# Kernel optimization log

Measured on AMD Instinct MI355X. Metric: run time of the kernel, lower is better.

## Reference

```python
import jax, jax.numpy as jnp
import numpy as np

TOP_K = 2

def setup_inputs() -> dict:
    key = jax.random.key(0)
    ks = jax.random.split(key, 8)
    B, S, H, E, F = 4, 2048, 1024, 8, 2048  # F = hidden * expansion(2)
    scale_in = 0.02
    return {
        "x": jax.random.normal(ks[0], (B, S, H), dtype=jnp.float32),
        "router_w": jax.random.normal(ks[1], (H, E), dtype=jnp.float32) * scale_in,
        "router_b": jnp.zeros((E,), dtype=jnp.float32),
        "w1": jax.random.normal(ks[2], (E, H, F), dtype=jnp.float32) * scale_in,
        "b1": jnp.zeros((E, F), dtype=jnp.float32),
        "w2": jax.random.normal(ks[3], (E, F, H), dtype=jnp.float32) * scale_in,
        "b2": jnp.zeros((E, H), dtype=jnp.float32),
    }

def reference(x, router_w, router_b, w1, b1, w2, b2):
    B, S, H = x.shape
    E = router_b.shape[0]
    T = B * S
    flat = x.reshape(T, H)
    # Router + top-k gating (softmax over the k selected logits, as in torch code)
    logits = flat @ router_w + router_b                       # [T, E]
    topk_scores, topk_idx = jax.lax.top_k(logits, TOP_K)      # [T, k]
    probs = jax.nn.softmax(topk_scores, axis=-1)              # [T, k]
    # Dense gate matrix: gates[t, e] = prob if e selected for token t else 0
    gates = jnp.zeros((T, E), dtype=flat.dtype).at[
        jnp.arange(T)[:, None], topk_idx
    ].add(probs)                                              # [T, E]
    # Expert FFNs computed as batched GEMMs over the expert axis
    h = jax.nn.relu(jnp.einsum('td,edf->etf', flat, w1) + b1[:, None, :])  # [E, T, F]
    eout = jnp.einsum('etf,efd->etd', h, w2) + b2[:, None, :]              # [E, T, H]
    out = jnp.einsum('etd,te->td', eout, gates)                            # [T, H]
    return out.reshape(B, S, H)
```

## Files before the change

### kernel.cpp

```cpp
#include <hip/hip_runtime.h>
#include <hip/hip_bf16.h>

#define T_TOK 8192
#define HDIM 1024
#define FDIM 2048
#define NEXP 8
#define NASSIGN (T_TOK * 2)
#define ROWCAP (NASSIGN + 128)
#define NHB 64

typedef __bf16 bf16;
typedef __bf16 bf16x4 __attribute__((ext_vector_type(4)));
typedef __bf16 bf16x8 __attribute__((ext_vector_type(8)));
typedef float f32x4 __attribute__((ext_vector_type(4)));

__device__ __forceinline__ void gload_lds16(const void* g, void* l) {
    __builtin_amdgcn_global_load_lds(
        (const __attribute__((address_space(1))) void*)(uintptr_t)g,
        (__attribute__((address_space(3))) void*)(uintptr_t)l,
        16, 0, 0);
}

__global__ __launch_bounds__(256) void transpose_to_bf16(
    const float* __restrict__ in, bf16* __restrict__ out, int R, int C) {
    __shared__ float tile[64][68];
    int e = blockIdx.z;
    const float* inp = in + (size_t)e * R * C;
    bf16* outp = out + (size_t)e * R * C;
    int c0 = blockIdx.x * 64, r0 = blockIdx.y * 64;
    int tid = threadIdx.x;
    int tx = tid & 15, ty = tid >> 4;
#pragma unroll
    for (int i = 0; i < 4; i++) {
        int row = ty + i * 16;
        float4 v = *(const float4*)&inp[(size_t)(r0 + row) * C + c0 + tx * 4];
        *(float4*)&tile[row][tx * 4] = v;
    }
    __syncthreads();
#pragma unroll
    for (int i = 0; i < 2; i++) {
        int idx = tid + i * 256;
        int c = idx >> 3, seg = idx & 7;
        bf16x8 v;
#pragma unroll
        for (int j = 0; j < 8; j++) v[j] = (bf16)tile[seg * 8 + j][c];
        *(bf16x8*)&outp[(size_t)(c0 + c) * R + r0 + seg * 8] = v;
    }
}

__global__ __launch_bounds__(256) void router_kernel(
    const float* __restrict__ x, const float* __restrict__ rw,
    const float* __restrict__ rb, int* __restrict__ expert_pair,
    float2* __restrict__ gate_pair) {
    __shared__ float rwT[NEXP][HDIM];
    __shared__ float rbs[NEXP];
    int tid = threadIdx.x;
    for (int i = tid; i < HDIM * NEXP / 4; i += 256) {
        float4 v = ((const float4*)rw)[i];
        int h = i >> 1, e0 = (i & 1) * 4;
        rwT[e0 + 0][h] = v.x;
        rwT[e0 + 1][h] = v.y;
        rwT[e0 + 2][h] = v.z;
        rwT[e0 + 3][h] = v.w;
    }
    if (tid < NEXP) rbs[tid] = rb[tid];
    __syncthreads();
    int wave = tid >> 6, lane = tid & 63;
    int tbase = blockIdx.x * 32 + wave * 8;

    for (int tk = 0; tk < 8; tk++) {
        int t = tbase + tk;
        const float4* xt = (const float4*)(x + (size_t)t * HDIM);
        float p[NEXP];
#pragma unroll
        for (int e = 0; e < NEXP; e++) p[e] = 0.f;
#pragma unroll
        for (int it = 0; it < 4; it++) {
            float4 v = xt[it * 64 + lane];
            int h = (it * 64 + lane) * 4;
#pragma unroll
            for (int e = 0; e < NEXP; e++) {
                float4 wv = *(const float4*)&rwT[e][h];
                p[e] += v.x * wv.x + v.y * wv.y + v.z * wv.z + v.w * wv.w;
            }
        }
#pragma unroll
        for (int off = 32; off >= 1; off >>= 1) {
#pragma unroll
            for (int e = 0; e < NEXP; e++) p[e] += __shfl_xor(p[e], off, 64);
        }
        if (lane == 0) {
            float lg[NEXP];
#pragma unroll
            for (int e = 0; e < NEXP; e++) lg[e] = p[e] + rbs[e];
            int e0 = 0;
#pragma unroll
            for (int e = 1; e < NEXP; e++)
                if (lg[e] > lg[e0]) e0 = e;
            int e1 = -1;
#pragma unroll
            for (int e = 0; e < NEXP; e++) {
                if (e == e0) continue;
                if (e1 < 0 || lg[e] > lg[e1]) e1 = e;
            }
            float z = expf(lg[e1] - lg[e0]);
            expert_pair[t] = e0 | (e1 << 16);
            gate_pair[t] = make_float2(1.f / (1.f + z), z / (1.f + z));
        }
    }
}

__global__ __launch_bounds__(256) void hist_kernel(
    const int* __restrict__ expert_pair, int* __restrict__ hist) {
    int tid = threadIdx.x;
    int wave = tid >> 6, lane = tid & 63;
    int a = blockIdx.x * 256 + tid;
    int t = a >> 1, j = a & 1;
    int e = (expert_pair[t] >> (16 * j)) & 0xffff;
    __shared__ int wcnt[4][NEXP];
#pragma unroll
    for (int ee = 0; ee < NEXP; ee++) {
        unsigned long long m = __ballot(e == ee);
        if (lane == 0) wcnt[wave][ee] = __popcll(m);
    }
    __syncthreads();
    if (tid < NEXP)
        hist[blockIdx.x * NEXP + tid] =
            wcnt[0][tid] + wcnt[1][tid] + wcnt[2][tid] + wcnt[3][tid];
}

__global__ __launch_bounds__(256) void scan_kernel(
    const int* __restrict__ hist, int* __restrict__ start,
    int* __restrict__ cnt, int* __restrict__ offs) {
    __shared__ int h[NHB * NEXP];
    __shared__ int tot[NEXP];
    __shared__ int offsh[NEXP];
    int tid = threadIdx.x;
    for (int i = tid; i < NHB * NEXP; i += 256) h[i] = hist[i];
    __syncthreads();
    if (tid < NEXP) {
        int s = 0;
        for (int b = 0; b < NHB; b++) s += h[b * NEXP + tid];
        tot[tid] = s;
        cnt[tid] = s;
    }
    __syncthreads();
    if (tid == 0) {
        int o = 0;
        for (int e = 0; e < NEXP; e++) {
            offsh[e] = o;
            offs[e] = o;
            o += tot[e];
        }
    }
    __syncthreads();
    if (tid < NEXP) {
        int run = offsh[tid];
        for (int b = 0; b < NHB; b++) {
            start[b * NEXP + tid] = run;
            run += h[b * NEXP + tid];
        }
    }
}

__global__ __launch_bounds__(256) void scatter_kernel(
    const int* __restrict__ expert_pair, const float2* __restrict__ gate_pair,
    const int* __restrict__ start, int* __restrict__ perm,
    float* __restrict__ gatebuf, int* __restrict__ rowbuf) {
    int tid = threadIdx.x;
    int wave = tid >> 6, lane = tid & 63;
    int a = blockIdx.x * 256 + tid;
    int t = a >> 1, j = a & 1;
    int e = (expert_pair[t] >> (16 * j)) & 0xffff;
    float2 gp = gate_pair[t];
    float g = j ? gp.y : gp.x;
    __shared__ int wcnt[4][NEXP];
    int rankw = 0;
    unsigned long long below = (1ull << lane) - 1ull;
#pragma unroll
    for (int ee = 0; ee < NEXP; ee++) {
        unsigned long long m = __ballot(e == ee);
        if (lane == 0) wcnt[wave][ee] = __popcll(m);
        if (ee == e) rankw = __popcll(m & below);
    }
    __syncthreads();
    int cross = 0;
    for (int w = 0; w < wave; w++) cross += wcnt[w][e];
    int pos = start[blockIdx.x * NEXP + e] + cross + rankw;
    perm[pos] = t;
    gatebuf[pos] = g;
    rowbuf[a] = pos;
}

__global__ __launch_bounds__(256) void pack_kernel(
    const float* __restrict__ x, const int* __restrict__ perm,
    bf16* __restrict__ xg) {
    int r0 = blockIdx.x * 16;
    int wave = threadIdx.x >> 6, lane = threadIdx.x & 63;
#pragma unroll
    for (int i = 0; i < 4; i++) {
        int row = r0 + wave * 4 + i;
        int tok = perm[row];
        const float* src = x + (size_t)tok * HDIM;
        bf16* dst = xg + (size_t)row * HDIM;
#pragma unroll
        for (int it = 0; it < 4; it++) {
            int c = (it * 64 + lane) * 4;
            float4 v = *(const float4*)&src[c];
            bf16x4 b = {(bf16)v.x, (bf16)v.y, (bf16)v.z, (bf16)v.w};
            *(bf16x4*)&dst[c] = b;
        }
    }
}

template <bool RELU, bool GATE>
__global__ __launch_bounds__(256) void moe_gemm(
    const bf16* __restrict__ A, const bf16* __restrict__ B,
    const float* __restrict__ bias, const float* __restrict__ gates,
    bf16* __restrict__ out, const int* __restrict__ cnt,
    const int* __restrict__ offs, int K, int N) {
    int e = blockIdx.z;
    int n_cnt = cnt[e];
    int m0 = blockIdx.y * 128;
    if (m0 >= n_cnt) return;
    int n0 = blockIdx.x * 128;

    __shared__ bf16 As[128 * 32];
    __shared__ bf16 Bs[128 * 32];

    int tid = threadIdx.x;
    int lane = tid & 63;
    int wave = tid >> 6;
    int wm = (wave & 1) * 64, wn = (wave >> 1) * 64;
    int quad = lane >> 4;
    int l16 = lane & 15;

    int off_e = offs[e];
    const bf16* Ae = A + (size_t)off_e * K;
    const bf16* Be = B + (size_t)e * N * K;

    int srow = lane >> 2;
    int scol = (lane & 3) ^ ((lane >> 2) & 3) ^ ((lane >> 4) & 3);
    const bf16* ag0 = Ae + (size_t)(m0 + wave * 16 + srow) * K + scol * 8;
    const bf16* ag1 = ag0 + (size_t)64 * K;
    const bf16* bg0 = Be + (size_t)(n0 + wave * 16 + srow) * K + scol * 8;
    const bf16* bg1 = bg0 + (size_t)64 * K;
    bf16* as0 = &As[(wave * 16) * 32];
    bf16* as1 = &As[(64 + wave * 16) * 32];
    bf16* bs0 = &Bs[(wave * 16) * 32];
    bf16* bs1 = &Bs[(64 + wave * 16) * 32];

    int dswz = (quad ^ (l16 & 3) ^ ((l16 >> 2) & 3)) * 8;

    f32x4 acc[4][4];
#pragma unroll
    for (int i = 0; i < 4; i++)
#pragma unroll
        for (int j = 0; j < 4; j++) acc[i][j] = f32x4{0.f, 0.f, 0.f, 0.f};

    for (int k0 = 0; k0 < K; k0 += 32) {
        gload_lds16(ag0 + k0, as0);
        gload_lds16(ag1 + k0, as1);
        gload_lds16(bg0 + k0, bs0);
        gload_lds16(bg1 + k0, bs1);
        __syncthreads();
        bf16x8 af[4], bfr[4];
#pragma unroll
        for (int i = 0; i < 4; i++)
            af[i] = *(const bf16x8*)&As[(wm + i * 16 + l16) * 32 + dswz];
#pragma unroll
        for (int j = 0; j < 4; j++)
            bfr[j] = *(const bf16x8*)&Bs[(wn + j * 16 + l16) * 32 + dswz];
#pragma unroll
        for (int i = 0; i < 4; i++)
#pragma unroll
            for (int j = 0; j < 4; j++)
                acc[i][j] = __builtin_amdgcn_mfma_f32_16x16x32_bf16(af[i], bfr[j], acc[i][j], 0, 0, 0);
        __syncthreads();
    }

#pragma unroll
    for (int i = 0; i < 4; i++)
#pragma unroll
        for (int j = 0; j < 4; j++)
#pragma unroll
            for (int r = 0; r < 4; r++) {
                int m = m0 + wm + i * 16 + quad * 4 + r;
                if (m < n_cnt) {
                    int n = n0 + wn + j * 16 + l16;
                    float v = acc[i][j][r] + bias[e * N + n];
                    if (RELU) v = v > 0.f ? v : 0.f;
                    if (GATE) v *= gates[off_e + m];
                    out[(size_t)(off_e + m) * N + n] = (bf16)v;
                }
            }
}

__global__ __launch_bounds__(256) void combine_kernel(
    const bf16* __restrict__ eout, const int* __restrict__ rowbuf,
    float* __restrict__ out) {
    int t = blockIdx.x;
    int r0 = rowbuf[2 * t], r1 = rowbuf[2 * t + 1];
    const bf16* p0 = eout + (size_t)r0 * HDIM;
    const bf16* p1 = eout + (size_t)r1 * HDIM;
    float* o = out + (size_t)t * HDIM;
    int n = threadIdx.x * 4;
    bf16x4 a = *(const bf16x4*)&p0[n];
    bf16x4 b = *(const bf16x4*)&p1[n];
    float4 v = {(float)a[0] + (float)b[0], (float)a[1] + (float)b[1],
                (float)a[2] + (float)b[2], (float)a[3] + (float)b[3]};
    *(float4*)&o[n] = v;
}

extern "C" void kernel_launch(void* const* d_in, const int* in_sizes, int n_in,
                              void* d_out, int out_size, void* d_ws, size_t ws_size,
                              hipStream_t stream) {
    const float* x = (const float*)d_in[0];
    const float* rw = (const float*)d_in[1];
    const float* rb = (const float*)d_in[2];
    const float* w1 = (const float*)d_in[3];
    const float* b1 = (const float*)d_in[4];
    const float* w2 = (const float*)d_in[5];
    const float* b2 = (const float*)d_in[6];
    float* out = (float*)d_out;

    char* ws = (char*)d_ws;
    size_t o = 0;
    auto alloc = [&](size_t bytes) {
        char* p = ws + o;
        o += (bytes + 255) & ~(size_t)255;
        return p;
    };
    bf16* w1t = (bf16*)alloc((size_t)NEXP * FDIM * HDIM * 2);
    bf16* w2t = (bf16*)alloc((size_t)NEXP * HDIM * FDIM * 2);
    bf16* hbuf = (bf16*)alloc((size_t)ROWCAP * FDIM * 2);
    bf16* xg = (bf16*)alloc((size_t)ROWCAP * HDIM * 2);
    bf16* eout = xg;
    int* expert_pair = (int*)alloc((size_t)T_TOK * 4);
    float2* gate_pair = (float2*)alloc((size_t)T_TOK * 8);
    int* hist = (int*)alloc((size_t)NHB * NEXP * 4);
    int* start = (int*)alloc((size_t)NHB * NEXP * 4);
    int* perm = (int*)alloc((size_t)NASSIGN * 4);
    float* gatebuf = (float*)alloc((size_t)NASSIGN * 4);
    int* rowbuf = (int*)alloc((size_t)NASSIGN * 4);
    int* cnt = (int*)alloc(256);
    int* offs = (int*)alloc(256);

    transpose_to_bf16<<<dim3(FDIM / 64, HDIM / 64, NEXP), 256, 0, stream>>>(w1, w1t, HDIM, FDIM);
    transpose_to_bf16<<<dim3(HDIM / 64, FDIM / 64, NEXP), 256, 0, stream>>>(w2, w2t, FDIM, HDIM);
    router_kernel<<<T_TOK / 32, 256, 0, stream>>>(x, rw, rb, expert_pair, gate_pair);
    hist_kernel<<<NHB, 256, 0, stream>>>(expert_pair, hist);
    scan_kernel<<<1, 256, 0, stream>>>(hist, start, cnt, offs);
    scatter_kernel<<<NHB, 256, 0, stream>>>(expert_pair, gate_pair, start, perm, gatebuf, rowbuf);
    pack_kernel<<<NASSIGN / 16, 256, 0, stream>>>(x, perm, xg);
    moe_gemm<true, false><<<dim3(FDIM / 128, T_TOK / 128, NEXP), 256, 0, stream>>>(
        xg, w1t, b1, nullptr, hbuf, cnt, offs, HDIM, FDIM);
    moe_gemm<false, true><<<dim3(HDIM / 128, T_TOK / 128, NEXP), 256, 0, stream>>>(
        hbuf, w2t, b2, gatebuf, eout, cnt, offs, FDIM, HDIM);
    combine_kernel<<<T_TOK, 256, 0, stream>>>(eout, rowbuf, out);
}
```

Measured before the change: 512.3 us.

## Double K-tile depth in MoE GEMM, interleave experts in grid, template K/N

The MoE grouped GEMM now stages 64-wide K slices in LDS instead of 32, with a new XOR swizzle over eight 16-byte chunks. Each barrier pair now covers two MFMA sub-steps, halving barrier and loop overhead per unit of work. The 3D grid becomes a 1D grid with the expert index in the low bits, so active blocks from different experts are spread across the launch instead of clustered. K and N become compile-time constants, and LDS use doubles, which may reduce occupancy.

Result: no change. 518.4 us (+1.2%).

```diff
diff --git a/kernel.cpp b/kernel.cpp
--- a/kernel.cpp
+++ b/kernel.cpp
@@ -8,6 +8,7 @@
 #define NASSIGN (T_TOK * 2)
 #define ROWCAP (NASSIGN + 128)
 #define NHB 64
+#define MT_MAX (T_TOK / 128)
 
 typedef __bf16 bf16;
 typedef __bf16 bf16x4 __attribute__((ext_vector_type(4)));
@@ -213,20 +214,24 @@
     }
 }
 
-template <bool RELU, bool GATE>
+template <int K, int N, bool RELU, bool GATE>
 __global__ __launch_bounds__(256) void moe_gemm(
     const bf16* __restrict__ A, const bf16* __restrict__ B,
     const float* __restrict__ bias, const float* __restrict__ gates,
     bf16* __restrict__ out, const int* __restrict__ cnt,
-    const int* __restrict__ offs, int K, int N) {
-    int e = blockIdx.z;
+    const int* __restrict__ offs) {
+    constexpr int NT = N / 128;
+    int lin = blockIdx.x;
+    int e = lin & 7;
+    int r = lin >> 3;
+    int nt = r % NT, mt = r / NT;
     int n_cnt = cnt[e];
-    int m0 = blockIdx.y * 128;
+    int m0 = mt * 128;
     if (m0 >= n_cnt) return;
-    int n0 = blockIdx.x * 128;
-
-    __shared__ bf16 As[128 * 32];
-    __shared__ bf16 Bs[128 * 32];
+    int n0 = nt * 128;
+
+    __shared__ bf16 As[128 * 64];
+    __shared__ bf16 Bs[128 * 64];
 
     int tid = threadIdx.x;
     int lane = tid & 63;
@@ -239,18 +244,21 @@
     const bf16* Ae = A + (size_t)off_e * K;
     const bf16* Be = B + (size_t)e * N * K;
 
-    int srow = lane >> 2;
-    int scol = (lane & 3) ^ ((lane >> 2) & 3) ^ ((lane >> 4) & 3);
-    const bf16* ag0 = Ae + (size_t)(m0 + wave * 16 + srow) * K + scol * 8;
-    const bf16* ag1 = ag0 + (size_t)64 * K;
-    const bf16* bg0 = Be + (size_t)(n0 + wave * 16 + srow) * K + scol * 8;
-    const bf16* bg1 = bg0 + (size_t)64 * K;
-    bf16* as0 = &As[(wave * 16) * 32];
-    bf16* as1 = &As[(64 + wave * 16) * 32];
-    bf16* bs0 = &Bs[(wave * 16) * 32];
-    bf16* bs1 = &Bs[(64 + wave * 16) * 32];
-
-    int dswz = (quad ^ (l16 & 3) ^ ((l16 >> 2) & 3)) * 8;
+    int srow8 = lane >> 3;
+    int ccol = ((lane & 7) ^ srow8) * 8;
+    const bf16* ag[4];
+    const bf16* bg[4];
+    bf16* asl[4];
+    bf16* bsl[4];
+#pragma unroll
+    for (int i = 0; i < 4; i++) {
+        int rowb = wave * 32 + i * 8;
+        ag[i] = Ae + (size_t)(m0 + rowb + srow8) * K + ccol;
+        bg[i] = Be + (size_t)(n0 + rowb + srow8) * K + ccol;
+        asl[i] = &As[rowb * 64];
+        bsl[i] = &Bs[rowb * 64];
+    }
+    int rchunk = l16 & 7;
 
     f32x4 acc[4][4];
 #pragma unroll
@@ -258,37 +266,43 @@
 #pragma unroll
         for (int j = 0; j < 4; j++) acc[i][j] = f32x4{0.f, 0.f, 0.f, 0.f};
 
-    for (int k0 = 0; k0 < K; k0 += 32) {
-        gload_lds16(ag0 + k0, as0);
-        gload_lds16(ag1 + k0, as1);
-        gload_lds16(bg0 + k0, bs0);
-        gload_lds16(bg1 + k0, bs1);
+#pragma unroll 1
+    for (int k0 = 0; k0 < K; k0 += 64) {
+#pragma unroll
+        for (int i = 0; i < 4; i++) {
+            gload_lds16(ag[i] + k0, asl[i]);
+            gload_lds16(bg[i] + k0, bsl[i]);
+        }
         __syncthreads();
-        bf16x8 af[4], bfr[4];
-#pragma unroll
-        for (int i = 0; i < 4; i++)
-            af[i] = *(const bf16x8*)&As[(wm + i * 16 + l16) * 32 + dswz];
+#pragma unroll
+        for (int s = 0; s < 2; s++) {
+            bf16x8 af[4], bfr[4];
+            int chnk = ((4 * s + quad) ^ rchunk) * 8;
+#pragma unroll
+            for (int i = 0; i < 4; i++)
+                af[i] = *(const bf16x8*)&As[(wm + i * 16 + l16) * 64 + chnk];
+#pragma unroll
+            for (int j = 0; j < 4; j++)
+                bfr[j] = *(const bf16x8*)&Bs[(wn + j * 16 + l16) * 64 + chnk];
+#pragma unroll
+            for (int i = 0; i < 4; i++)
+#pragma unroll
+                for (int j = 0; j < 4; j++)
+                    acc[i][j] = __builtin_amdgcn_mfma_f32_16x16x32_bf16(af[i], bfr[j], acc[i][j], 0, 0, 0);
+        }
+        __syncthreads();
+    }
+
+#pragma unroll
+    for (int i = 0; i < 4; i++)
 #pragma unroll
         for (int j = 0; j < 4; j++)
-            bfr[j] = *(const bf16x8*)&Bs[(wn + j * 16 + l16) * 32 + dswz];
-#pragma unroll
-        for (int i = 0; i < 4; i++)
-#pragma unroll
-            for (int j = 0; j < 4; j++)
-                acc[i][j] = __builtin_amdgcn_mfma_f32_16x16x32_bf16(af[i], bfr[j], acc[i][j], 0, 0, 0);
-        __syncthreads();
-    }
-
-#pragma unroll
-    for (int i = 0; i < 4; i++)
-#pragma unroll
-        for (int j = 0; j < 4; j++)
-#pragma unroll
-            for (int r = 0; r < 4; r++) {
-                int m = m0 + wm + i * 16 + quad * 4 + r;
+#pragma unroll
+            for (int rr = 0; rr < 4; rr++) {
+                int m = m0 + wm + i * 16 + quad * 4 + rr;
                 if (m < n_cnt) {
                     int n = n0 + wn + j * 16 + l16;
-                    float v = acc[i][j][r] + bias[e * N + n];
+                    float v = acc[i][j][rr] + bias[e * N + n];
                     if (RELU) v = v > 0.f ? v : 0.f;
                     if (GATE) v *= gates[off_e + m];
                     out[(size_t)(off_e + m) * N + n] = (bf16)v;
@@ -353,9 +367,9 @@
     scan_kernel<<<1, 256, 0, stream>>>(hist, start, cnt, offs);
     scatter_kernel<<<NHB, 256, 0, stream>>>(expert_pair, gate_pair, start, perm, gatebuf, rowbuf);
     pack_kernel<<<NASSIGN / 16, 256, 0, stream>>>(x, perm, xg);
-    moe_gemm<true, false><<<dim3(FDIM / 128, T_TOK / 128, NEXP), 256, 0, stream>>>(
-        xg, w1t, b1, nullptr, hbuf, cnt, offs, HDIM, FDIM);
-    moe_gemm<false, true><<<dim3(HDIM / 128, T_TOK / 128, NEXP), 256, 0, stream>>>(
-        hbuf, w2t, b2, gatebuf, eout, cnt, offs, FDIM, HDIM);
+    moe_gemm<HDIM, FDIM, true, false><<<NEXP * (FDIM / 128) * MT_MAX, 256, 0, stream>>>(
+        xg, w1t, b1, nullptr, hbuf, cnt, offs);
+    moe_gemm<FDIM, HDIM, false, true><<<NEXP * (HDIM / 128) * MT_MAX, 256, 0, stream>>>(
+        hbuf, w2t, b2, gatebuf, eout, cnt, offs);
     combine_kernel<<<T_TOK, 256, 0, stream>>>(eout, rowbuf, out);
 }
```
